# Kernel optimization log

Measured on AMD Instinct MI355X. Metric: run time of the kernel, lower is better.

Reference implementation:

```python
import jax, jax.numpy as jnp
import numpy as np

B, S, H, D = 4, 1024, 32, 128   # batch, seq_len, heads, head_dim (prefill path, past_len=0)
HID = H * D                      # 4096
L, R = 8, 16                     # num_loras, lora rank
SCALE = 1.0 / float(np.sqrt(D))
LORA_SCALE = 1.0
ROPE_BASE = 10000.0


def setup_inputs() -> dict:
    key = jax.random.key(0)
    ks = jax.random.split(key, 16)
    T = B * S
    inp = {
        "x": jax.random.normal(ks[0], (T, HID), dtype=jnp.float32),
        "lora_idx": jax.random.randint(ks[1], (T,), 0, L, dtype=jnp.int32),
    }
    for i, n in enumerate(["Wq", "Wk", "Wv", "Wo"]):
        inp[n] = jax.random.normal(ks[2 + i], (HID, HID), dtype=jnp.float32) * 0.02
    for i, p in enumerate(["q", "k", "v", "o"]):
        inp[f"wa_{p}"] = jax.random.normal(ks[6 + 2 * i], (L, R, HID), dtype=jnp.float32) * 0.02
        inp[f"wb_{p}"] = jax.random.normal(ks[7 + 2 * i], (L, HID, R), dtype=jnp.float32) * 0.02
    return inp


def _add_lora(x, wa, wb, onehot):
    # punica bgmv: per-token lora: scale * (x @ A[idx]^T) @ B[idx]^T
    # Computed via one-hot selection to avoid materializing [T, O, R] gathers.
    a = jnp.einsum('th,lrh->tlr', x, wa)          # [T, L, R] (tiny)
    a_sel = jnp.einsum('tlr,tl->tr', a, onehot)   # [T, R]
    ar = jnp.einsum('tr,tl->tlr', a_sel, onehot)  # route back through lora slot
    return jnp.einsum('tlr,lor->to', ar, wb)      # [T, O]


def _rotary(x, cos, sin):
    # rotate_half over full head_dim: [-x2, x1]
    half = jnp.concatenate([-x[..., D // 2:], x[..., :D // 2]], axis=-1)
    return x * cos + half * sin


def reference(x, lora_idx, Wq, Wk, Wv, Wo,
              wa_q, wb_q, wa_k, wb_k, wa_v, wb_v, wa_o, wb_o):
    onehot = jax.nn.one_hot(lora_idx, L, dtype=x.dtype)  # [T, L]

    q = x @ Wq.T + LORA_SCALE * _add_lora(x, wa_q, wb_q, onehot)
    k = x @ Wk.T + LORA_SCALE * _add_lora(x, wa_k, wb_k, onehot)
    v = x @ Wv.T + LORA_SCALE * _add_lora(x, wa_v, wb_v, onehot)

    # [T, HID] -> [B, H, S, D]
    qh = q.reshape(B, S, H, D).transpose(0, 2, 1, 3)
    kh = k.reshape(B, S, H, D).transpose(0, 2, 1, 3)
    vh = v.reshape(B, S, H, D).transpose(0, 2, 1, 3)

    # rotary embedding, positions beg=past_len=0 .. S-1
    pos = jnp.arange(S, dtype=x.dtype)
    inv_freq = 1.0 / (ROPE_BASE ** (jnp.arange(0, D, 2, dtype=jnp.float32) / D)).astype(x.dtype)
    freqs = pos[:, None] * inv_freq[None, :]           # [S, D/2]
    emb = jnp.concatenate([freqs, freqs], axis=-1)     # [S, D]
    cos = jnp.cos(emb)[None, None]                     # [1,1,S,D]
    sin = jnp.sin(emb)[None, None]
    qh = _rotary(qh, cos, sin)
    kh = _rotary(kh, cos, sin)

    # causal SDPA
    scores = jnp.einsum('bhqd,bhkd->bhqk', qh, kh) * SCALE
    causal = jnp.tril(jnp.ones((S, S), dtype=bool))
    scores = jnp.where(causal[None, None], scores, jnp.finfo(scores.dtype).min)
    probs = jax.nn.softmax(scores, axis=-1)
    attn = jnp.einsum('bhqk,bhkd->bhqd', probs, vh)    # [B,H,S,D]
    attn = attn.transpose(0, 2, 1, 3).reshape(B * S, HID)

    out = attn @ Wo.T + LORA_SCALE * _add_lora(attn, wa_o, wb_o, onehot)
    return out
```

## Files before the change

### kernel.cpp

```cpp
#include <hip/hip_runtime.h>

#define HIDN 4096
#define KEXT 4224
#define TTOK 4096
#define SEQL 1024
#define NB 4
#define NHEAD 32
#define SCALEF 0.08838834764831845f

typedef __attribute__((ext_vector_type(8))) short bf16x8;
typedef __attribute__((ext_vector_type(8))) unsigned short u16x8;
typedef __attribute__((ext_vector_type(4))) float f32x4;

static __device__ __forceinline__ unsigned short f2bf(float f) {
  union { float f; unsigned u; } v; v.f = f;
  unsigned r = v.u + 0x7fffu + ((v.u >> 16) & 1u);
  return (unsigned short)(r >> 16);
}
static __device__ __forceinline__ void load_lds16(const void* g, void* l) {
  __builtin_amdgcn_global_load_lds((const __attribute__((address_space(1))) void*)g,
                                   (__attribute__((address_space(3))) void*)l, 16, 0, 0);
}

__global__ __launch_bounds__(256) void f2b_kernel(const float* __restrict__ s,
                                                  unsigned short* __restrict__ d) {
  size_t i = ((size_t)blockIdx.x * 256 + threadIdx.x) * 4;
  float4 v = *(const float4*)(s + i);
  ushort4 o;
  o.x = f2bf(v.x); o.y = f2bf(v.y); o.z = f2bf(v.z); o.w = f2bf(v.w);
  *(ushort4*)(d + i) = o;
}

__global__ __launch_bounds__(256) void f2b_pad_kernel(const float* __restrict__ s,
                                                      unsigned short* __restrict__ d) {
  size_t i = ((size_t)blockIdx.x * 256 + threadIdx.x) * 4;
  int row = (int)(i >> 12);
  int col = (int)(i & 4095);
  float4 v = *(const float4*)(s + i);
  ushort4 o;
  o.x = f2bf(v.x); o.y = f2bf(v.y); o.z = f2bf(v.z); o.w = f2bf(v.w);
  *(ushort4*)(d + (size_t)row * KEXT + col) = o;
}

__global__ __launch_bounds__(256) void conv_w_kernel(const float* __restrict__ W,
    const float* __restrict__ wb, unsigned short* __restrict__ wext) {
  int bid = blockIdx.x;
  if (bid < 16384) {
    size_t i = ((size_t)bid * 256 + threadIdx.x) * 4;
    int row = (int)(i >> 12);
    int col = (int)(i & 4095);
    float4 v = *(const float4*)(W + i);
    ushort4 o;
    o.x = f2bf(v.x); o.y = f2bf(v.y); o.z = f2bf(v.z); o.w = f2bf(v.w);
    *(ushort4*)(wext + (size_t)row * KEXT + col) = o;
  } else {
    int idx = (bid - 16384) * 256 + threadIdx.x;
    int o = idx >> 5;
    int j4 = (idx & 31) * 4;
    int l = j4 >> 4, r = j4 & 15;
    float4 v = *(const float4*)(wb + ((size_t)l * HIDN + o) * 16 + r);
    ushort4 q;
    q.x = f2bf(v.x); q.y = f2bf(v.y); q.z = f2bf(v.z); q.w = f2bf(v.w);
    *(ushort4*)(wext + (size_t)o * KEXT + 4096 + j4) = q;
  }
}

__global__ __launch_bounds__(256) void conv_wa3_kernel(const float* __restrict__ s0,
    const float* __restrict__ s1, const float* __restrict__ s2,
    unsigned short* __restrict__ d) {
  int sel = blockIdx.x >> 9;
  const float* s = (sel == 0) ? s0 : ((sel == 1) ? s1 : s2);
  size_t i = ((size_t)(blockIdx.x & 511) * 256 + threadIdx.x) * 4;
  float4 v = *(const float4*)(s + i);
  ushort4 o;
  o.x = f2bf(v.x); o.y = f2bf(v.y); o.z = f2bf(v.z); o.w = f2bf(v.w);
  *(ushort4*)(d + (size_t)sel * 128 * HIDN + i) = o;
}

__global__ __launch_bounds__(128) void afat_kernel(const float* __restrict__ afull, int aoff,
    int awidth, const int* __restrict__ lidx, unsigned short* __restrict__ xext) {
  int t = blockIdx.x, j = threadIdx.x;
  int l = lidx[t];
  float v = afull[(size_t)t * awidth + aoff + j];
  unsigned short o = ((j >> 4) == l) ? f2bf(v) : (unsigned short)0;
  xext[(size_t)t * KEXT + 4096 + j] = o;
}

__global__ __launch_bounds__(256) void rope_tab_kernel(float* __restrict__ cosb,
                                                       float* __restrict__ sinb) {
  int i = blockIdx.x * 256 + threadIdx.x;
  int s = i >> 6, j = i & 63;
  float inv = __expf(-__logf(10000.0f) * (float)j * (1.0f / 64.0f));
  float f = (float)s * inv;
  cosb[i] = cosf(f);
  sinb[i] = sinf(f);
}

template<int BUF, bool ST>
__device__ __forceinline__ void ktile(char* lds, f32x4 (&acc)[8][4], int a_rd, int b_rd,
    const unsigned short* aS0, const unsigned short* aS1,
    const unsigned short* bS0, const unsigned short* bS1, int stg, int kn) {
  const int NB_ = (BUF ^ 1) * 32768;
  bf16x8 bfr[4];
  {
    __builtin_amdgcn_sched_barrier(0);
    bf16x8 af[4];
    #pragma unroll
    for (int mi = 0; mi < 4; ++mi)
      af[mi] = *(const bf16x8*)(lds + BUF * 32768 + a_rd + mi * 1024);
    #pragma unroll
    for (int ni = 0; ni < 4; ++ni)
      bfr[ni] = *(const bf16x8*)(lds + 65536 + BUF * 32768 + b_rd + (ni & 1) * 1024 + (ni >> 1) * 4096);
    if (ST) {
      load_lds16(aS0 + kn, lds + NB_ + stg);
      load_lds16(aS1 + kn, lds + NB_ + stg + 1024);
    }
    __builtin_amdgcn_s_setprio(1);
    #pragma unroll
    for (int mi = 0; mi < 4; ++mi)
      #pragma unroll
      for (int ni = 0; ni < 4; ++ni)
        acc[mi][ni] = __builtin_amdgcn_mfma_f32_16x16x32_bf16(af[mi], bfr[ni], acc[mi][ni], 0, 0, 0);
    __builtin_amdgcn_s_setprio(0);
  }
  {
    __builtin_amdgcn_sched_barrier(0);
    bf16x8 af[4];
    #pragma unroll
    for (int mi = 0; mi < 4; ++mi)
      af[mi] = *(const bf16x8*)(lds + BUF * 32768 + 4096 + a_rd + mi * 1024);
    if (ST) {
      load_lds16(bS0 + kn, lds + 65536 + NB_ + stg);
      load_lds16(bS1 + kn, lds + 65536 + NB_ + stg + 1024);
    }
    __builtin_amdgcn_s_setprio(1);
    #pragma unroll
    for (int mi = 0; mi < 4; ++mi)
      #pragma unroll
      for (int ni = 0; ni < 4; ++ni)
        acc[4 + mi][ni] = __builtin_amdgcn_mfma_f32_16x16x32_bf16(af[mi], bfr[ni], acc[4 + mi][ni], 0, 0, 0);
    __builtin_amdgcn_s_setprio(0);
  }
  if (ST) asm volatile("s_waitcnt vmcnt(4)" ::: "memory");
  else    asm volatile("s_waitcnt vmcnt(0)" ::: "memory");
  __builtin_amdgcn_s_barrier();
  {
    __builtin_amdgcn_sched_barrier(0);
    bf16x8 af[4];
    #pragma unroll
    for (int mi = 0; mi < 4; ++mi)
      af[mi] = *(const bf16x8*)(lds + BUF * 32768 + 16384 + a_rd + mi * 1024);
    #pragma unroll
    for (int ni = 0; ni < 4; ++ni)
      bfr[ni] = *(const bf16x8*)(lds + 65536 + BUF * 32768 + 16384 + b_rd + (ni & 1) * 1024 + (ni >> 1) * 4096);
    if (ST) {
      load_lds16(aS0 + kn + 32, lds + NB_ + 16384 + stg);
      load_lds16(aS1 + kn + 32, lds + NB_ + 16384 + stg + 1024);
    }
    __builtin_amdgcn_s_setprio(1);
    #pragma unroll
    for (int mi = 0; mi < 4; ++mi)
      #pragma unroll
      for (int ni = 0; ni < 4; ++ni)
        acc[mi][ni] = __builtin_amdgcn_mfma_f32_16x16x32_bf16(af[mi], bfr[ni], acc[mi][ni], 0, 0, 0);
    __builtin_amdgcn_s_setprio(0);
  }
  {
    __builtin_amdgcn_sched_barrier(0);
    bf16x8 af[4];
    #pragma unroll
    for (int mi = 0; mi < 4; ++mi)
      af[mi] = *(const bf16x8*)(lds + BUF * 32768 + 16384 + 4096 + a_rd + mi * 1024);
    if (ST) {
      load_lds16(bS0 + kn + 32, lds + 65536 + NB_ + 16384 + stg);
      load_lds16(bS1 + kn + 32, lds + 65536 + NB_ + 16384 + stg + 1024);
    }
    __builtin_amdgcn_s_setprio(1);
    #pragma unroll
    for (int mi = 0; mi < 4; ++mi)
      #pragma unroll
      for (int ni = 0; ni < 4; ++ni)
        acc[4 + mi][ni] = __builtin_amdgcn_mfma_f32_16x16x32_bf16(af[mi], bfr[ni], acc[4 + mi][ni], 0, 0, 0);
    __builtin_amdgcn_s_setprio(0);
  }
  if (ST) {
    asm volatile("s_waitcnt vmcnt(4)" ::: "memory");
    __builtin_amdgcn_s_barrier();
  }
}

template<int KTOT, int MODE>
__global__ __launch_bounds__(512, 2) void gemm256_kernel(const unsigned short* __restrict__ A,
    const unsigned short* __restrict__ Bw, void* __restrict__ Cout,
    const float* __restrict__ cosb, const float* __restrict__ sinb) {
  extern __shared__ char lds[];
  const int K = KTOT;
  int tid = threadIdx.x, lane = tid & 63, wave = tid >> 6;
  int wm = wave >> 2, wn = wave & 3;
  int l15 = lane & 15, l16 = lane >> 4;
  int orig = blockIdx.y * 16 + blockIdx.x;
  int swz = (orig & 7) * 32 + (orig >> 3);
  int bm = (swz >> 4) * 256, bn = (swz & 15) * 256;
  int srA0 = (wave * 2 + 0) * 16 + (lane >> 2);
  int srA1 = (wave * 2 + 1) * 16 + (lane >> 2);
  int scA0 = ((lane & 3) ^ ((srA0 >> 1) & 3)) * 8;
  int scA1 = ((lane & 3) ^ ((srA1 >> 1) & 3)) * 8;
  const unsigned short* aS0 = A + (size_t)(bm + srA0) * K + scA0;
  const unsigned short* aS1 = A + (size_t)(bm + srA1) * K + scA1;
  const unsigned short* bS0 = Bw + (size_t)(bn + srA0) * K + scA0;
  const unsigned short* bS1 = Bw + (size_t)(bn + srA1) * K + scA1;
  int stg = wave * 2048 + lane * 16;
  int rslot = (l16 ^ ((l15 >> 1) & 3)) * 16;
  int a_rd = (wm * 128 + l15) * 64 + rslot;
  int wcbase = (wn >> 1) * 128 + (wn & 1) * 32;
  int b_rd = (wcbase + l15) * 64 + rslot;
  f32x4 acc[8][4];
  const f32x4 fz = {0.f, 0.f, 0.f, 0.f};
  #pragma unroll
  for (int i = 0; i < 8; ++i)
    #pragma unroll
    for (int j = 0; j < 4; ++j) acc[i][j] = fz;
  load_lds16(aS0, lds + stg);
  load_lds16(aS1, lds + stg + 1024);
  load_lds16(bS0, lds + 65536 + stg);
  load_lds16(bS1, lds + 65536 + stg + 1024);
  load_lds16(aS0 + 32, lds + 16384 + stg);
  load_lds16(aS1 + 32, lds + 16384 + stg + 1024);
  load_lds16(bS0 + 32, lds + 65536 + 16384 + stg);
  load_lds16(bS1 + 32, lds + 65536 + 16384 + stg + 1024);
  asm volatile("s_waitcnt vmcnt(4)" ::: "memory");
  __builtin_amdgcn_s_barrier();
  for (int tt = 0; tt < KTOT / 128 - 1; ++tt) {
    ktile<0, true>(lds, acc, a_rd, b_rd, aS0, aS1, bS0, bS1, stg, (2 * tt + 1) * 64);
    ktile<1, true>(lds, acc, a_rd, b_rd, aS0, aS1, bS0, bS1, stg, (2 * tt + 2) * 64);
  }
  ktile<0, true>(lds, acc, a_rd, b_rd, aS0, aS1, bS0, bS1, stg, (KTOT / 64 - 1) * 64);
  ktile<1, false>(lds, acc, a_rd, b_rd, aS0, aS1, bS0, bS1, stg, 0);

  if (MODE == 0) {
    float* C = (float*)Cout;
    #pragma unroll
    for (int mi = 0; mi < 8; ++mi) {
      int gr = bm + wm * 128 + mi * 16 + l16 * 4;
      #pragma unroll
      for (int ni = 0; ni < 4; ++ni) {
        int gc = bn + wcbase + (ni & 1) * 16 + (ni >> 1) * 64 + l15;
        #pragma unroll
        for (int r = 0; r < 4; ++r)
          C[(size_t)(gr + r) * HIDN + gc] = acc[mi][ni][r];
      }
    }
  } else if (MODE == 2) {
    unsigned short* O = (unsigned short*)Cout;
    #pragma unroll
    for (int mi = 0; mi < 8; ++mi) {
      int gr = bm + wm * 128 + mi * 16 + l16 * 4;
      #pragma unroll
      for (int ni = 0; ni < 4; ++ni) {
        int gc = bn + wcbase + (ni & 1) * 16 + (ni >> 1) * 64 + l15;
        #pragma unroll
        for (int r = 0; r < 4; ++r)
          O[(size_t)(gr + r) * HIDN + gc] = f2bf(acc[mi][ni][r]);
      }
    }
  } else {
    unsigned short* O = (unsigned short*)Cout;
    #pragma unroll
    for (int mi = 0; mi < 8; ++mi) {
      int gr = bm + wm * 128 + mi * 16 + l16 * 4;
      #pragma unroll
      for (int p = 0; p < 2; ++p) {
        int jj = (wn & 1) * 32 + p * 16 + l15;
        int gclo = bn + wcbase + p * 16 + l15;
        #pragma unroll
        for (int r = 0; r < 4; ++r) {
          int row = gr + r;
          int s = row & (SEQL - 1);
          float cs = cosb[s * 64 + jj];
          float sn = sinb[s * 64 + jj];
          float lo = acc[mi][p][r], hi = acc[mi][p + 2][r];
          O[(size_t)row * HIDN + gclo] = f2bf(lo * cs - hi * sn);
          O[(size_t)row * HIDN + gclo + 64] = f2bf(hi * cs + lo * sn);
        }
      }
    }
  }
}

__global__ __launch_bounds__(256) void gemm_bt_splitk_kernel(const unsigned short* __restrict__ A,
    const unsigned short* __restrict__ Bw, float* __restrict__ Cp, int N, int Ka) {
  __shared__ __align__(16) unsigned short As[128][32];
  __shared__ __align__(16) unsigned short Bs[128][32];
  const int KSPAN = 512;
  int tid = threadIdx.x;
  int lane = tid & 63, wave = tid >> 6;
  int bm = blockIdx.y * 128, bn = blockIdx.x * 128;
  int k0 = blockIdx.z * KSPAN;
  int wr = (wave >> 1) * 64, wc = (wave & 1) * 64;
  const f32x4 fz = {0.f, 0.f, 0.f, 0.f};
  f32x4 acc[4][4];
  #pragma unroll
  for (int i = 0; i < 4; ++i)
    #pragma unroll
    for (int j = 0; j < 4; ++j) acc[i][j] = fz;
  const unsigned short* a0 = A + (size_t)(bm + (tid >> 2)) * Ka + (tid & 3) * 8 + k0;
  const unsigned short* b0 = Bw + (size_t)(bn + (tid >> 2)) * HIDN + (tid & 3) * 8 + k0;
  char* lA = (char*)&As[0][0] + wave * 1024;
  char* lB = (char*)&Bs[0][0] + wave * 1024;
  int l15 = lane & 15, l4 = (lane >> 4) * 8;
  for (int kt = 0; kt < KSPAN; kt += 32) {
    load_lds16(a0 + kt, lA);
    load_lds16(a0 + kt + (size_t)64 * Ka, lA + 4096);
    load_lds16(b0 + kt, lB);
    load_lds16(b0 + kt + (size_t)64 * HIDN, lB + 4096);
    __syncthreads();
    bf16x8 af[4], bfr[4];
    #pragma unroll
    for (int mi = 0; mi < 4; ++mi) af[mi] = *(const bf16x8*)&As[wr + mi * 16 + l15][l4];
    #pragma unroll
    for (int ni = 0; ni < 4; ++ni) bfr[ni] = *(const bf16x8*)&Bs[wc + ni * 16 + l15][l4];
    #pragma unroll
    for (int mi = 0; mi < 4; ++mi)
      #pragma unroll
      for (int ni = 0; ni < 4; ++ni)
        acc[mi][ni] = __builtin_amdgcn_mfma_f32_16x16x32_bf16(af[mi], bfr[ni], acc[mi][ni], 0, 0, 0);
    __syncthreads();
  }
  float* Cz = Cp + (size_t)blockIdx.z * TTOK * N;
  #pragma unroll
  for (int mi = 0; mi < 4; ++mi) {
    int r0 = bm + wr + mi * 16 + (lane >> 4) * 4;
    #pragma unroll
    for (int ni = 0; ni < 4; ++ni) {
      int c = bn + wc + ni * 16 + l15;
      #pragma unroll
      for (int r = 0; r < 4; ++r)
        Cz[(size_t)(r0 + r) * N + c] = acc[mi][ni][r];
    }
  }
}

__global__ __launch_bounds__(256) void reduce8_kernel(const float* __restrict__ Cp,
                                                      float* __restrict__ C, int n) {
  int i = (blockIdx.x * 256 + threadIdx.x) * 4;
  float4 s = *(const float4*)(Cp + i);
  #pragma unroll
  for (int z = 1; z < 8; ++z) {
    float4 v = *(const float4*)(Cp + (size_t)z * n + i);
    s.x += v.x; s.y += v.y; s.z += v.z; s.w += v.w;
  }
  *(float4*)(C + i) = s;
}

__global__ __launch_bounds__(256) void attn_kernel(const unsigned short* __restrict__ qb,
    const unsigned short* __restrict__ kb, const unsigned short* __restrict__ vb,
    unsigned short* __restrict__ ob) {
  __shared__ __align__(16) unsigned short Ks[2][32][128];
  __shared__ __align__(16) unsigned short Vt[128][40];
  __shared__ __align__(16) unsigned short Ps[4][16][40];
  int tid = threadIdx.x, lane = tid & 63, wave = tid >> 6;
  int id = blockIdx.y * gridDim.x + blockIdx.x;
  int xcd = id & 7, w = id >> 3;
  int bh = xcd * 16 + (w & 15);
  int qt = 15 - (w >> 4);
  int b = bh >> 5, h = bh & 31;
  size_t base = ((size_t)b * SEQL) * HIDN + (size_t)h * 128;
  size_t obase = ((size_t)b * SEQL) * KEXT + (size_t)h * 128;
  int l15 = lane & 15, l16 = lane >> 4;
  int krow = tid >> 4;
  int kslot = (tid & 15) ^ (krow & 7);
  const unsigned short* kgbase = kb + base + (size_t)krow * HIDN + kslot * 8;
  char* lK0 = (char*)&Ks[0][0][0] + wave * 1024;
  char* lK1 = (char*)&Ks[1][0][0] + wave * 1024;
  int vd = tid >> 1;
  int vks0 = (tid & 1) * 2;
  const unsigned short* vgbase = vb + base + vd;
  char* vtp = (char*)&Vt[0][0] + vd * 80 + vks0 * 16;
  const f32x4 fz = {0.f, 0.f, 0.f, 0.f};
  const short ONEBF = (short)0x3F80;
  const bf16x8 ones = {ONEBF, ONEBF, ONEBF, ONEBF, ONEBF, ONEBF, ONEBF, ONEBF};

  int q0 = qt * 64;
  int kend = q0 + 64;
  int qrow = q0 + wave * 16 + l15;
  const unsigned short* qrp = qb + base + (size_t)qrow * HIDN + l16 * 8;
  bf16x8 qf[4];
  #pragma unroll
  for (int ks = 0; ks < 4; ++ks) qf[ks] = *(const bf16x8*)(qrp + ks * 32);
  f32x4 oacc[8];
  #pragma unroll
  for (int i = 0; i < 8; ++i) oacc[i] = fz;
  f32x4 sumac = fz;
  load_lds16(kgbase, lK0);
  load_lds16(kgbase + (size_t)16 * HIDN, lK0 + 4096);
  {
    bf16x8 v0, v1;
    const unsigned short* vg = vgbase + (size_t)(vks0 * 8) * HIDN;
    #pragma unroll
    for (int j = 0; j < 8; ++j) v0[j] = (short)vg[(size_t)j * HIDN];
    #pragma unroll
    for (int j = 0; j < 8; ++j) v1[j] = (short)vg[(size_t)(8 + j) * HIDN];
    *(bf16x8*)vtp = v0;
    *(bf16x8*)(vtp + 16) = v1;
  }
  __syncthreads();
  for (int kt = 0; kt < kend; kt += 32) {
    int cur = (kt >> 5) & 1;
    int more = (kt + 32) < kend;
    bf16x8 nv0, nv1;
    if (more) {
      char* lKn = cur ? lK0 : lK1;
      load_lds16(kgbase + (size_t)(kt + 32) * HIDN, lKn);
      load_lds16(kgbase + (size_t)(kt + 48) * HIDN, lKn + 4096);
      const unsigned short* vg = vgbase + (size_t)(kt + 32 + vks0 * 8) * HIDN;
      #pragma unroll
      for (int j = 0; j < 8; ++j) nv0[j] = (short)vg[(size_t)j * HIDN];
      #pragma unroll
      for (int j = 0; j < 8; ++j) nv1[j] = (short)vg[(size_t)(8 + j) * HIDN];
    }
    const char* ksb = (const char*)&Ks[cur][0][0];
    f32x4 sacc[2] = {fz, fz};
    #pragma unroll
    for (int ks = 0; ks < 4; ++ks) {
      #pragma unroll
      for (int nf = 0; nf < 2; ++nf) {
        int row = nf * 16 + l15;
        int slot = (ks * 4 + l16) ^ (l15 & 7);
        bf16x8 kf = *(const bf16x8*)(ksb + row * 256 + slot * 16);
        sacc[nf] = __builtin_amdgcn_mfma_f32_16x16x32_bf16(qf[ks], kf, sacc[nf], 0, 0, 0);
      }
    }
    if (kt + 31 <= q0 + wave * 16) {
      #pragma unroll
      for (int rr = 0; rr < 4; ++rr) {
        float e0 = __expf(SCALEF * sacc[0][rr]);
        float e1 = __expf(SCALEF * sacc[1][rr]);
        Ps[wave][l16 * 4 + rr][l15] = f2bf(e0);
        Ps[wave][l16 * 4 + rr][16 + l15] = f2bf(e1);
      }
    } else {
      #pragma unroll
      for (int rr = 0; rr < 4; ++rr) {
        int qr = q0 + wave * 16 + l16 * 4 + rr;
        float e0 = (kt + l15 > qr) ? 0.f : __expf(SCALEF * sacc[0][rr]);
        float e1 = (kt + 16 + l15 > qr) ? 0.f : __expf(SCALEF * sacc[1][rr]);
        Ps[wave][l16 * 4 + rr][l15] = f2bf(e0);
        Ps[wave][l16 * 4 + rr][16 + l15] = f2bf(e1);
      }
    }
    bf16x8 pf = *(const bf16x8*)&Ps[wave][l15][l16 * 8];
    sumac = __builtin_amdgcn_mfma_f32_16x16x32_bf16(pf, ones, sumac, 0, 0, 0);
    #pragma unroll
    for (int nf = 0; nf < 8; ++nf) {
      bf16x8 vf = *(const bf16x8*)((const char*)&Vt[0][0] + (nf * 16 + l15) * 80 + l16 * 16);
      oacc[nf] = __builtin_amdgcn_mfma_f32_16x16x32_bf16(pf, vf, oacc[nf], 0, 0, 0);
    }
    __syncthreads();
    if (more) {
      *(bf16x8*)vtp = nv0;
      *(bf16x8*)(vtp + 16) = nv1;
    }
    __syncthreads();
  }
  #pragma unroll
  for (int rr = 0; rr < 4; ++rr) {
    int qr = q0 + wave * 16 + l16 * 4 + rr;
    float inv = 1.0f / sumac[rr];
    unsigned short* orow = ob + obase + (size_t)qr * KEXT;
    #pragma unroll
    for (int nf = 0; nf < 8; ++nf)
      orow[nf * 16 + l15] = f2bf(oacc[nf][rr] * inv);
  }
}

extern "C" void kernel_launch(void* const* d_in, const int* in_sizes, int n_in,
                              void* d_out, int out_size, void* d_ws, size_t ws_size,
                              hipStream_t stream) {
  (void)in_sizes; (void)n_in; (void)out_size; (void)ws_size;
  const float* x = (const float*)d_in[0];
  const int* lidx = (const int*)d_in[1];
  const float* W[4] = {(const float*)d_in[2], (const float*)d_in[3],
                       (const float*)d_in[4], (const float*)d_in[5]};
  const float* wa_q = (const float*)d_in[6];
  const float* wb_q = (const float*)d_in[7];
  const float* wa_k = (const float*)d_in[8];
  const float* wb_k = (const float*)d_in[9];
  const float* wa_v = (const float*)d_in[10];
  const float* wb_v = (const float*)d_in[11];
  const float* wa_o = (const float*)d_in[12];
  const float* wb_o = (const float*)d_in[13];
  float* out = (float*)d_out;

  char* p = (char*)d_ws;
  unsigned short* Xext = (unsigned short*)p;  p += (size_t)TTOK * KEXT * 2;
  unsigned short* Wext = (unsigned short*)p;  p += (size_t)HIDN * KEXT * 2;
  float* tmp = (float*)p;                     p += (size_t)TTOK * HIDN * 4;
  unsigned short* qbuf = (unsigned short*)p;  p += (size_t)TTOK * HIDN * 2;
  unsigned short* kbuf = (unsigned short*)p;  p += (size_t)TTOK * HIDN * 2;
  unsigned short* vbuf = (unsigned short*)p;  p += (size_t)TTOK * HIDN * 2;
  unsigned short* Aext = (unsigned short*)p;  p += (size_t)TTOK * KEXT * 2;
  unsigned short* WAbf = (unsigned short*)p;  p += (size_t)384 * HIDN * 2;
  float* afull = (float*)p;                   p += (size_t)TTOK * 384 * 4;
  float* aofull = (float*)p;                  p += (size_t)TTOK * 128 * 4;
  float* cosb = (float*)p;                    p += (size_t)SEQL * 64 * 4;
  float* sinb = (float*)p;                    p += (size_t)SEQL * 64 * 4;

  const int CVT_BLOCKS = (TTOK * HIDN) / 1024;
  const int CVT_WA = (128 * HIDN) / 1024;
  const int CONVW_BLOCKS = CVT_BLOCKS + (HIDN * 32) / 256;
  dim3 g256(16, 16);

  hipFuncSetAttribute((const void*)gemm256_kernel<KEXT, 0>,
                      hipFuncAttributeMaxDynamicSharedMemorySize, 131072);
  hipFuncSetAttribute((const void*)gemm256_kernel<KEXT, 1>,
                      hipFuncAttributeMaxDynamicSharedMemorySize, 131072);
  hipFuncSetAttribute((const void*)gemm256_kernel<KEXT, 2>,
                      hipFuncAttributeMaxDynamicSharedMemorySize, 131072);

  rope_tab_kernel<<<(SEQL * 64) / 256, 256, 0, stream>>>(cosb, sinb);
  f2b_pad_kernel<<<CVT_BLOCKS, 256, 0, stream>>>(x, Xext);
  conv_wa3_kernel<<<3 * CVT_WA, 256, 0, stream>>>(wa_q, wa_k, wa_v, WAbf);
  gemm_bt_splitk_kernel<<<dim3(3, 32, 8), 256, 0, stream>>>(Xext, WAbf, tmp, 384, KEXT);
  reduce8_kernel<<<(TTOK * 384) / 1024, 256, 0, stream>>>(tmp, afull, TTOK * 384);

  conv_w_kernel<<<CONVW_BLOCKS, 256, 0, stream>>>(W[0], wb_q, Wext);
  afat_kernel<<<TTOK, 128, 0, stream>>>(afull, 0, 384, lidx, Xext);
  gemm256_kernel<KEXT, 1><<<g256, 512, 131072, stream>>>(Xext, Wext, qbuf, cosb, sinb);
  conv_w_kernel<<<CONVW_BLOCKS, 256, 0, stream>>>(W[1], wb_k, Wext);
  afat_kernel<<<TTOK, 128, 0, stream>>>(afull, 128, 384, lidx, Xext);
  gemm256_kernel<KEXT, 1><<<g256, 512, 131072, stream>>>(Xext, Wext, kbuf, cosb, sinb);
  conv_w_kernel<<<CONVW_BLOCKS, 256, 0, stream>>>(W[2], wb_v, Wext);
  afat_kernel<<<TTOK, 128, 0, stream>>>(afull, 256, 384, lidx, Xext);
  gemm256_kernel<KEXT, 2><<<g256, 512, 131072, stream>>>(Xext, Wext, vbuf, nullptr, nullptr);

  attn_kernel<<<dim3(8, 256), 256, 0, stream>>>(qbuf, kbuf, vbuf, Aext);

  f2b_kernel<<<CVT_WA, 256, 0, stream>>>(wa_o, WAbf);
  gemm_bt_splitk_kernel<<<dim3(1, 32, 8), 256, 0, stream>>>(Aext, WAbf, tmp, 128, KEXT);
  reduce8_kernel<<<(TTOK * 128) / 1024, 256, 0, stream>>>(tmp, aofull, TTOK * 128);
  conv_w_kernel<<<CONVW_BLOCKS, 256, 0, stream>>>(W[3], wb_o, Wext);
  afat_kernel<<<TTOK, 128, 0, stream>>>(aofull, 0, 128, lidx, Aext);
  gemm256_kernel<KEXT, 0><<<g256, 512, 131072, stream>>>(Aext, Wext, out, nullptr, nullptr);
}
```

Baseline: 796.9 us.

## Prefetch V two tiles ahead in attention with manual waitcnt barriers

The attention loop is unrolled by two with ping-pong register buffers, so the transposed V rows are loaded two key tiles ahead rather than one. The __syncthreads calls become inline s_waitcnt/s_barrier with a partial vmcnt, so outstanding V loads can stay in flight across the barrier, and sched_barrier fences keep the load issue order fixed. This aims to hide global-load latency behind the MFMA work, at the cost of more live registers and correctness that depends on the hand-written waitcnt counts.

```diff
diff --git a/kernel.cpp b/kernel.cpp
--- a/kernel.cpp
+++ b/kernel.cpp
@@ -352,6 +352,67 @@
   *(float4*)(C + i) = s;
 }
 
+#define ATTN_STEP(T, CUR, W0, W1, L0, L1)                                              \
+  {                                                                                    \
+    const int haveK = (T) + 32 < kend;                                                 \
+    const int haveV2 = (T) + 64 < kend;                                                \
+    if (haveK) {                                                                       \
+      char* lKn = (CUR) ? lK0 : lK1;                                                   \
+      load_lds16(kgbase + (size_t)((T) + 32) * HIDN, lKn);                             \
+      load_lds16(kgbase + (size_t)((T) + 48) * HIDN, lKn + 4096);                      \
+    }                                                                                  \
+    __builtin_amdgcn_sched_barrier(0);                                                 \
+    if (haveV2) {                                                                      \
+      const unsigned short* vg = vgbase + (size_t)((T) + 64 + vks0 * 8) * HIDN;        \
+      for (int j = 0; j < 8; ++j) L0[j] = (short)vg[(size_t)j * HIDN];                 \
+      for (int j = 0; j < 8; ++j) L1[j] = (short)vg[(size_t)(8 + j) * HIDN];           \
+    }                                                                                  \
+    __builtin_amdgcn_sched_barrier(0);                                                 \
+    const char* ksb = (const char*)&Ks[CUR][0][0];                                     \
+    f32x4 sacc[2] = {fz, fz};                                                          \
+    for (int ks = 0; ks < 4; ++ks) {                                                   \
+      for (int nf = 0; nf < 2; ++nf) {                                                 \
+        int row = nf * 16 + l15;                                                       \
+        int slot = (ks * 4 + l16) ^ (l15 & 7);                                         \
+        bf16x8 kf = *(const bf16x8*)(ksb + row * 256 + slot * 16);                     \
+        sacc[nf] = __builtin_amdgcn_mfma_f32_16x16x32_bf16(qf[ks], kf, sacc[nf], 0, 0, 0); \
+      }                                                                                \
+    }                                                                                  \
+    if ((T) + 31 <= q0 + wave * 16) {                                                  \
+      for (int rr = 0; rr < 4; ++rr) {                                                 \
+        float e0 = __expf(SCALEF * sacc[0][rr]);                                       \
+        float e1 = __expf(SCALEF * sacc[1][rr]);                                       \
+        Ps[wave][l16 * 4 + rr][l15] = f2bf(e0);                                        \
+        Ps[wave][l16 * 4 + rr][16 + l15] = f2bf(e1);                                   \
+      }                                                                                \
+    } else {                                                                           \
+      for (int rr = 0; rr < 4; ++rr) {                                                 \
+        int qr = q0 + wave * 16 + l16 * 4 + rr;                                        \
+        float e0 = ((T) + l15 > qr) ? 0.f : __expf(SCALEF * sacc[0][rr]);              \
+        float e1 = ((T) + 16 + l15 > qr) ? 0.f : __expf(SCALEF * sacc[1][rr]);         \
+        Ps[wave][l16 * 4 + rr][l15] = f2bf(e0);                                        \
+        Ps[wave][l16 * 4 + rr][16 + l15] = f2bf(e1);                                   \
+      }                                                                                \
+    }                                                                                  \
+    bf16x8 pf = *(const bf16x8*)&Ps[wave][l15][l16 * 8];                               \
+    sumac = __builtin_amdgcn_mfma_f32_16x16x32_bf16(pf, ones, sumac, 0, 0, 0);         \
+    for (int nf = 0; nf < 8; ++nf) {                                                   \
+      bf16x8 vf = *(const bf16x8*)((const char*)&Vt[0][0] + (nf * 16 + l15) * 80 + l16 * 16); \
+      oacc[nf] = __builtin_amdgcn_mfma_f32_16x16x32_bf16(pf, vf, oacc[nf], 0, 0, 0);   \
+    }                                                                                  \
+    asm volatile("s_waitcnt lgkmcnt(0)\n\ts_barrier" ::: "memory");                    \
+    if (haveK) {                                                                       \
+      *(bf16x8*)vtp = W0;                                                              \
+      *(bf16x8*)(vtp + 16) = W1;                                                       \
+    }                                                                                  \
+    if (haveV2)                                                                        \
+      asm volatile("s_waitcnt lgkmcnt(0) vmcnt(16)\n\ts_barrier" ::: "memory");        \
+    else if (haveK)                                                                    \
+      asm volatile("s_waitcnt lgkmcnt(0) vmcnt(0)\n\ts_barrier" ::: "memory");         \
+    else                                                                               \
+      asm volatile("s_waitcnt lgkmcnt(0)\n\ts_barrier" ::: "memory");                  \
+  }
+
 __global__ __launch_bounds__(256) void attn_kernel(const unsigned short* __restrict__ qb,
     const unsigned short* __restrict__ kb, const unsigned short* __restrict__ vb,
     unsigned short* __restrict__ ob) {
@@ -403,64 +464,18 @@
     *(bf16x8*)vtp = v0;
     *(bf16x8*)(vtp + 16) = v1;
   }
+  bf16x8 nA0, nA1, nB0, nB1;
+  {
+    const unsigned short* vg = vgbase + (size_t)(32 + vks0 * 8) * HIDN;
+    #pragma unroll
+    for (int j = 0; j < 8; ++j) nA0[j] = (short)vg[(size_t)j * HIDN];
+    #pragma unroll
+    for (int j = 0; j < 8; ++j) nA1[j] = (short)vg[(size_t)(8 + j) * HIDN];
+  }
   __syncthreads();
-  for (int kt = 0; kt < kend; kt += 32) {
-    int cur = (kt >> 5) & 1;
-    int more = (kt + 32) < kend;
-    bf16x8 nv0, nv1;
-    if (more) {
-      char* lKn = cur ? lK0 : lK1;
-      load_lds16(kgbase + (size_t)(kt + 32) * HIDN, lKn);
-      load_lds16(kgbase + (size_t)(kt + 48) * HIDN, lKn + 4096);
-      const unsigned short* vg = vgbase + (size_t)(kt + 32 + vks0 * 8) * HIDN;
-      #pragma unroll
-      for (int j = 0; j < 8; ++j) nv0[j] = (short)vg[(size_t)j * HIDN];
-      #pragma unroll
-      for (int j = 0; j < 8; ++j) nv1[j] = (short)vg[(size_t)(8 + j) * HIDN];
-    }
-    const char* ksb = (const char*)&Ks[cur][0][0];
-    f32x4 sacc[2] = {fz, fz};
-    #pragma unroll
-    for (int ks = 0; ks < 4; ++ks) {
-      #pragma unroll
-      for (int nf = 0; nf < 2; ++nf) {
-        int row = nf * 16 + l15;
-        int slot = (ks * 4 + l16) ^ (l15 & 7);
-        bf16x8 kf = *(const bf16x8*)(ksb + row * 256 + slot * 16);
-        sacc[nf] = __builtin_amdgcn_mfma_f32_16x16x32_bf16(qf[ks], kf, sacc[nf], 0, 0, 0);
-      }
-    }
-    if (kt + 31 <= q0 + wave * 16) {
-      #pragma unroll
-      for (int rr = 0; rr < 4; ++rr) {
-        float e0 = __expf(SCALEF * sacc[0][rr]);
-        float e1 = __expf(SCALEF * sacc[1][rr]);
-        Ps[wave][l16 * 4 + rr][l15] = f2bf(e0);
-        Ps[wave][l16 * 4 + rr][16 + l15] = f2bf(e1);
-      }
-    } else {
-      #pragma unroll
-      for (int rr = 0; rr < 4; ++rr) {
-        int qr = q0 + wave * 16 + l16 * 4 + rr;
-        float e0 = (kt + l15 > qr) ? 0.f : __expf(SCALEF * sacc[0][rr]);
-        float e1 = (kt + 16 + l15 > qr) ? 0.f : __expf(SCALEF * sacc[1][rr]);
-        Ps[wave][l16 * 4 + rr][l15] = f2bf(e0);
-        Ps[wave][l16 * 4 + rr][16 + l15] = f2bf(e1);
-      }
-    }
-    bf16x8 pf = *(const bf16x8*)&Ps[wave][l15][l16 * 8];
-    sumac = __builtin_amdgcn_mfma_f32_16x16x32_bf16(pf, ones, sumac, 0, 0, 0);
-    #pragma unroll
-    for (int nf = 0; nf < 8; ++nf) {
-      bf16x8 vf = *(const bf16x8*)((const char*)&Vt[0][0] + (nf * 16 + l15) * 80 + l16 * 16);
-      oacc[nf] = __builtin_amdgcn_mfma_f32_16x16x32_bf16(pf, vf, oacc[nf], 0, 0, 0);
-    }
-    __syncthreads();
-    if (more) {
-      *(bf16x8*)vtp = nv0;
-      *(bf16x8*)(vtp + 16) = nv1;
-    }
-    __syncthreads();
+  for (int kt = 0; kt < kend; kt += 64) {
+    ATTN_STEP(kt, 0, nA0, nA1, nB0, nB1);
+    ATTN_STEP(kt + 32, 1, nB0, nB1, nA0, nA1);
   }
   #pragma unroll
   for (int rr = 0; rr < 4; ++rr) {
```

Result: no change. 790.3 us (median of 2 runs) (-0.8%).
